# Kernel tuning notes

Measured on AMD Instinct MI355X. Metric: run time of the kernel, lower is better.

## Reference

```python
import jax, jax.numpy as jnp
import numpy as np

T, B, D, H = 1024, 64, 128, 256


def setup_inputs() -> dict:
    key = jax.random.key(0)
    ks = jax.random.split(key, 12)
    k = 1.0 / np.sqrt(H)  # torch LSTMCell init bound
    u = lambda kk, shape: jax.random.uniform(kk, shape, jnp.float32, -k, k)
    inputs = jax.random.normal(ks[0], (T, B, D), jnp.float32)
    hx = jnp.zeros((2, B, H), jnp.float32)
    cx = jnp.zeros((2, B, H), jnp.float32)
    return {
        'inputs': inputs, 'hx': hx, 'cx': cx,
        'Wih_f': u(ks[1], (4 * H, D)), 'Whh_f': u(ks[2], (4 * H, H)),
        'bih_f': u(ks[3], (4 * H,)), 'bhh_f': u(ks[4], (4 * H,)),
        'Wih_r': u(ks[5], (4 * H, D)), 'Whh_r': u(ks[6], (4 * H, H)),
        'bih_r': u(ks[7], (4 * H,)), 'bhh_r': u(ks[8], (4 * H,)),
    }


def _lstm_scan(x, h0, c0, Wih, Whh, bih, bhh, reverse):
    # Batch all input projections up front: [T,B,4H]
    gx = jnp.einsum('tbd,gd->tbg', x, Wih) + (bih + bhh)

    def step(carry, g):
        h, c = carry
        gates = g + h @ Whh.T  # [B,4H]
        i, f, gg, o = jnp.split(gates, 4, axis=-1)  # torch gate order i,f,g,o
        i = jax.nn.sigmoid(i)
        f = jax.nn.sigmoid(f)
        gg = jnp.tanh(gg)
        o = jax.nn.sigmoid(o)
        c = f * c + i * gg
        h = o * jnp.tanh(c)
        return (h, c), h

    # reverse=True scans back-to-front but emits outputs in original time
    # order, matching flip -> loop -> flip in the torch code.
    (h, c), ys = jax.lax.scan(step, (h0, c0), gx, reverse=reverse)
    return ys, h, c


def reference(inputs, hx, cx, Wih_f, Whh_f, bih_f, bhh_f,
              Wih_r, Whh_r, bih_r, bhh_r):
    yf, hf, cf = _lstm_scan(inputs, hx[0], cx[0], Wih_f, Whh_f, bih_f, bhh_f, False)
    yr, hr, cr = _lstm_scan(inputs, hx[1], cx[1], Wih_r, Whh_r, bih_r, bhh_r, True)
    out = jnp.concatenate([yf, yr], axis=-1)  # [T,B,2H]
    hy = jnp.stack([hf, hr], 0)  # [2,B,H]
    cy = jnp.stack([cf, cr], 0)
    return out, hy, cy
```

## Files before the change

### kernel.cpp

```cpp
#include <hip/hip_runtime.h>
#include <cstddef>

#define T_STEPS 1024
#define NB      64
#define DIN     128
#define HID     256
#define WPG     16

typedef unsigned short u16;
typedef unsigned int   u32;
typedef unsigned long long u64;
typedef __attribute__((ext_vector_type(8))) short short8;
typedef __attribute__((ext_vector_type(4))) float f32x4;

#define WG_OFF   0u
#define BIAS_OFF 1572864u
#define XB_OFF   1581056u
#define HB_OFF   18358272u
#define FL_OFF   18489344u

#define OUT_MAIN (T_STEPS * NB * 2 * HID)
#define TAIL_H   OUT_MAIN
#define TAIL_C   (OUT_MAIN + 2 * NB * HID)

__device__ __forceinline__ u16 f2bf(float f) {
  unsigned u = __float_as_uint(f);
  return (u16)((u + 0x7fffu + ((u >> 16) & 1u)) >> 16);
}
__device__ __forceinline__ float sigm(float v) { return 1.f / (1.f + __expf(-v)); }
__device__ __forceinline__ float tanh_fast(float x) {
  float e = __expf(-2.f * fabsf(x));
  float r = (1.f - e) / (1.f + e);
  return x < 0.f ? -r : r;
}

__global__ void prep_kernel(const float* __restrict__ x,
                            const float* __restrict__ Wih_f, const float* __restrict__ Whh_f,
                            const float* __restrict__ bih_f, const float* __restrict__ bhh_f,
                            const float* __restrict__ Wih_r, const float* __restrict__ Whh_r,
                            const float* __restrict__ bih_r, const float* __restrict__ bhh_r,
                            const float* __restrict__ hx,
                            u16* __restrict__ Wg, float* __restrict__ bias4,
                            u16* __restrict__ xb, u16* __restrict__ hbuf,
                            u32* __restrict__ flags) {
  const int total = 786432 + 2048 + 8388608 + 32768 + 8192;
  for (int i = blockIdx.x * blockDim.x + threadIdx.x; i < total;
       i += gridDim.x * blockDim.x) {
    if (i < 786432) {
      int d = i / 393216;
      int r = i - d * 393216;
      int rowg = r / 384, k = r - rowg * 384;
      int j = rowg >> 2, q = rowg & 3;
      int g = q * HID + j;
      const float* Wih = d ? Wih_r : Wih_f;
      const float* Whh = d ? Whh_r : Whh_f;
      float v = (k < DIN) ? Wih[g * DIN + k] : Whh[g * HID + (k - DIN)];
      Wg[i] = f2bf(v);
    } else if (i < 786432 + 2048) {
      int r = i - 786432;
      int d = r >> 10, rowg = r & 1023;
      int j = rowg >> 2, q = rowg & 3;
      int g = q * HID + j;
      bias4[r] = d ? (bih_r[g] + bhh_r[g]) : (bih_f[g] + bhh_f[g]);
    } else if (i < 786432 + 2048 + 8388608) {
      int r = i - (786432 + 2048);
      xb[r] = f2bf(x[r]);
    } else if (i < 786432 + 2048 + 8388608 + 32768) {
      int r = i - (786432 + 2048 + 8388608);
      int d = r >> 14, b = (r >> 8) & 63, j = r & 255;
      int grp = d * 4 + (b >> 4), bb = b & 15;
      hbuf[((size_t)(8 + grp) * 16 + bb) * 256 + j] = f2bf(hx[r]);
      hbuf[((size_t)(0 + grp) * 16 + bb) * 256 + j] = 0;
    } else {
      int r = i - (786432 + 2048 + 8388608 + 32768);
      flags[r] = ((r & 1023) == 0) ? (u32)WPG : 0u;
    }
  }
}

#define MFMA __builtin_amdgcn_mfma_f32_16x16x32_bf16
#define ALD64(P) __hip_atomic_load((P), __ATOMIC_RELAXED, __HIP_MEMORY_SCOPE_AGENT)

__global__ __launch_bounds__(256, 1) void lstm_flag(
    const u16* __restrict__ Wg, const float* __restrict__ bias4,
    const u16* __restrict__ xb, const float* __restrict__ cx,
    u16* __restrict__ hbuf, u32* __restrict__ flags,
    float* __restrict__ out) {
  extern __shared__ char smem[];
  u16* wl   = (u16*)smem;
  u16* xsh  = (u16*)(smem + 50176);
  u16* hsh  = (u16*)(smem + 58880);
  float* gl = (float*)(smem + 67328);

  const int tid = threadIdx.x;
  const int bid = blockIdx.x;
  const int grp = bid & 7;
  const int jsl = bid >> 3;
  const int d = grp >> 2, b0 = (grp & 3) * 16;
  const int w = tid >> 6, l = tid & 63;

  {
    const u32* src = (const u32*)(Wg + (size_t)(d * 1024 + jsl * 64) * 384);
    u32* dst = (u32*)wl;
    for (int iu = tid; iu < 64 * 192; iu += 256) {
      int r = iu / 192, c = iu - r * 192;
      dst[r * 196 + c] = src[iu];
    }
  }
  const float bv = bias4[d * 1024 + jsl * 64 + w * 16 + (l & 15)];

  const int eb = tid >> 4, ej = tid & 15;
  const int jglob = jsl * 16 + ej;
  float c_reg = cx[((size_t)d * NB + b0 + eb) * HID + jglob];

  const int xr_row = tid >> 4;
  const int xc = (tid & 15) * 8;
  const int pb = tid >> 4;
  const int cj0 = (tid & 15) * 16;

  { int t0 = d ? 1023 : 0;
    *(uint4*)&xsh[(0 * 16 + xr_row) * 136 + xc] =
        *(const uint4*)&xb[((size_t)t0 * NB + b0 + xr_row) * DIN + xc]; }
  uint4 xv;
  { int t1 = d ? 1022 : 1;
    xv = *(const uint4*)&xb[((size_t)t1 * NB + b0 + xr_row) * DIN + xc]; }
  u64 h0, h1, h2, h3;
  { const u64* hp = (const u64*)(hbuf + ((size_t)(8 + grp) * 16 + pb) * 256 + cj0);
    h0 = ALD64(hp + 0); h1 = ALD64(hp + 1); h2 = ALD64(hp + 2); h3 = ALD64(hp + 3); }
  __syncthreads();

  for (int s = 0; s < T_STEPS; ++s) {
    const int p = s & 1;
    const int t = d ? (1023 - s) : s;

    if (s < 1023) *(uint4*)&xsh[((p ^ 1) * 16 + xr_row) * 136 + xc] = xv;

    f32x4 acc = {bv, bv, bv, bv};
    {
      const u16* xr = &xsh[(p * 16 + (l & 15)) * 136 + (l >> 4) * 8];
      const u16* wr = wl + (size_t)(w * 16 + (l & 15)) * 392 + (l >> 4) * 8;
      acc = MFMA(*(const short8*)(xr + 0),  *(const short8*)(wr + 0),  acc, 0, 0, 0);
      acc = MFMA(*(const short8*)(xr + 32), *(const short8*)(wr + 32), acc, 0, 0, 0);
      acc = MFMA(*(const short8*)(xr + 64), *(const short8*)(wr + 64), acc, 0, 0, 0);
      acc = MFMA(*(const short8*)(xr + 96), *(const short8*)(wr + 96), acc, 0, 0, 0);
    }
    {
      uint4 H0, H1;
      H0.x = (u32)h0; H0.y = (u32)(h0 >> 32); H0.z = (u32)h1; H0.w = (u32)(h1 >> 32);
      H1.x = (u32)h2; H1.y = (u32)(h2 >> 32); H1.z = (u32)h3; H1.w = (u32)(h3 >> 32);
      *(uint4*)&hsh[pb * 264 + cj0] = H0;
      *(uint4*)&hsh[pb * 264 + cj0 + 8] = H1;
    }
    asm volatile("s_waitcnt lgkmcnt(0)" ::: "memory");
    __builtin_amdgcn_s_barrier();

    {
      const u16* hr = &hsh[(l & 15) * 264 + (l >> 4) * 8];
      const u16* wr = wl + (size_t)(w * 16 + (l & 15)) * 392 + 128 + (l >> 4) * 8;
#pragma unroll
      for (int kb = 0; kb < 8; ++kb)
        acc = MFMA(*(const short8*)(hr + 32 * kb), *(const short8*)(wr + 32 * kb),
                   acc, 0, 0, 0);
    }
    {
      int n = w * 16 + (l & 15);
      int m0 = (l >> 4) * 4;
      gl[(m0 + 0) * 68 + n] = acc[0]; gl[(m0 + 1) * 68 + n] = acc[1];
      gl[(m0 + 2) * 68 + n] = acc[2]; gl[(m0 + 3) * 68 + n] = acc[3];
    }
    asm volatile("s_waitcnt lgkmcnt(0)" ::: "memory");
    __builtin_amdgcn_s_barrier();

    f32x4 g4 = *(const f32x4*)&gl[eb * 68 + 4 * ej];
    float ii = sigm(g4[0]), ff = sigm(g4[1]);
    float gg = tanh_fast(g4[2]), oo = sigm(g4[3]);
    float c = ff * c_reg + ii * gg;
    c_reg = c;
    float h = oo * tanh_fast(c);
    u16 hb16 = f2bf(h);
    __hip_atomic_store(hbuf + ((size_t)(p * 8 + grp) * 16 + eb) * 256 + jglob,
                       hb16, __ATOMIC_RELAXED, __HIP_MEMORY_SCOPE_AGENT);
    asm volatile("s_waitcnt vmcnt(0)" ::: "memory");
    __builtin_amdgcn_s_barrier();
    if (tid == 0 && s < 1023)
      __hip_atomic_fetch_add(flags + grp * 1024 + (s + 1), 1u,
                             __ATOMIC_RELAXED, __HIP_MEMORY_SCOPE_AGENT);
    out[((size_t)t * NB + b0 + eb) * (2 * HID) + d * HID + jglob] = h;
    if (s == 1023) {
      out[TAIL_H + ((size_t)d * NB + b0 + eb) * HID + jglob] = h;
      out[TAIL_C + ((size_t)d * NB + b0 + eb) * HID + jglob] = c;
    }
    if (s < 1022) {
      int tn = d ? (1021 - s) : (s + 2);
      xv = *(const uint4*)&xb[((size_t)tn * NB + b0 + xr_row) * DIN + xc];
    }
    if (s < 1023) {
      if (tid == 0) {
        const u32* fp = flags + grp * 1024 + (s + 1);
        while (__hip_atomic_load(fp, __ATOMIC_RELAXED, __HIP_MEMORY_SCOPE_AGENT) < WPG)
          __builtin_amdgcn_s_sleep(1);
      }
      __builtin_amdgcn_s_barrier();
      const u64* hp = (const u64*)(hbuf + ((size_t)(p * 8 + grp) * 16 + pb) * 256 + cj0);
      h0 = ALD64(hp + 0); h1 = ALD64(hp + 1); h2 = ALD64(hp + 2); h3 = ALD64(hp + 3);
    }
  }
}

extern "C" void kernel_launch(void* const* d_in, const int* in_sizes, int n_in,
                              void* d_out, int out_size, void* d_ws, size_t ws_size,
                              hipStream_t stream) {
  const float* x     = (const float*)d_in[0];
  const float* hx    = (const float*)d_in[1];
  const float* cx    = (const float*)d_in[2];
  const float* Wih_f = (const float*)d_in[3];
  const float* Whh_f = (const float*)d_in[4];
  const float* bih_f = (const float*)d_in[5];
  const float* bhh_f = (const float*)d_in[6];
  const float* Wih_r = (const float*)d_in[7];
  const float* Whh_r = (const float*)d_in[8];
  const float* bih_r = (const float*)d_in[9];
  const float* bhh_r = (const float*)d_in[10];
  float* out = (float*)d_out;

  u16* Wg      = (u16*)((char*)d_ws + WG_OFF);
  float* bias4 = (float*)((char*)d_ws + BIAS_OFF);
  u16* xb      = (u16*)((char*)d_ws + XB_OFF);
  u16* hbuf    = (u16*)((char*)d_ws + HB_OFF);
  u32* flags   = (u32*)((char*)d_ws + FL_OFF);

  hipFuncSetAttribute((const void*)lstm_flag,
                      hipFuncAttributeMaxDynamicSharedMemorySize, 86016);

  hipLaunchKernelGGL(prep_kernel, dim3(2048), dim3(256), 0, stream,
                     x, Wih_f, Whh_f, bih_f, bhh_f, Wih_r, Whh_r, bih_r, bhh_r,
                     hx, Wg, bias4, xb, hbuf, flags);
  hipLaunchKernelGGL(lstm_flag, dim3(128), dim3(256), 86016, stream,
                     Wg, bias4, xb, cx, hbuf, flags, out);
}
```

Measured before the change: 2.167 ms.

## Replace flag-counter barrier with step-tagged hidden-state messages in 4-slot ring

Drops the per-step atomic counter flag and its spin-wait by packing a 16-bit step tag next to each bf16 hidden value in a 32-bit word. Consumers poll the tagged values directly from a 4-deep ring buffer and re-read any word whose tag is stale. The gate activation now runs per wave on its own slice of the LDS scratch, which removes one block barrier per step. MFMA accumulation is split into two chains for ILP. The cost is twice the hbuf traffic and a busy-poll loop with no sleep.

```diff
diff --git a/kernel.cpp b/kernel.cpp
--- a/kernel.cpp
+++ b/kernel.cpp
@@ -5,7 +5,6 @@
 #define NB      64
 #define DIN     128
 #define HID     256
-#define WPG     16
 
 typedef unsigned short u16;
 typedef unsigned int   u32;
@@ -17,7 +16,6 @@
 #define BIAS_OFF 1572864u
 #define XB_OFF   1581056u
 #define HB_OFF   18358272u
-#define FL_OFF   18489344u
 
 #define OUT_MAIN (T_STEPS * NB * 2 * HID)
 #define TAIL_H   OUT_MAIN
@@ -41,9 +39,8 @@
                             const float* __restrict__ bih_r, const float* __restrict__ bhh_r,
                             const float* __restrict__ hx,
                             u16* __restrict__ Wg, float* __restrict__ bias4,
-                            u16* __restrict__ xb, u16* __restrict__ hbuf,
-                            u32* __restrict__ flags) {
-  const int total = 786432 + 2048 + 8388608 + 32768 + 8192;
+                            u16* __restrict__ xb, u32* __restrict__ hbuf) {
+  const int total = 786432 + 2048 + 8388608 + 131072;
   for (int i = blockIdx.x * blockDim.x + threadIdx.x; i < total;
        i += gridDim.x * blockDim.x) {
     if (i < 786432) {
@@ -65,27 +62,31 @@
     } else if (i < 786432 + 2048 + 8388608) {
       int r = i - (786432 + 2048);
       xb[r] = f2bf(x[r]);
-    } else if (i < 786432 + 2048 + 8388608 + 32768) {
+    } else {
       int r = i - (786432 + 2048 + 8388608);
-      int d = r >> 14, b = (r >> 8) & 63, j = r & 255;
-      int grp = d * 4 + (b >> 4), bb = b & 15;
-      hbuf[((size_t)(8 + grp) * 16 + bb) * 256 + j] = f2bf(hx[r]);
-      hbuf[((size_t)(0 + grp) * 16 + bb) * 256 + j] = 0;
-    } else {
-      int r = i - (786432 + 2048 + 8388608 + 32768);
-      flags[r] = ((r & 1023) == 0) ? (u32)WPG : 0u;
+      int slot = r >> 15;
+      int rem  = r & 32767;
+      int grp = rem >> 12, bb = (rem >> 8) & 15, j = r & 255;
+      if (slot == 3) {
+        int d = grp >> 2, b = (grp & 3) * 16 + bb;
+        hbuf[r] = (1u << 16) | f2bf(hx[((size_t)d * NB + b) * HID + j]);
+      } else {
+        hbuf[r] = 0u;
+      }
     }
   }
 }
 
 #define MFMA __builtin_amdgcn_mfma_f32_16x16x32_bf16
 #define ALD64(P) __hip_atomic_load((P), __ATOMIC_RELAXED, __HIP_MEMORY_SCOPE_AGENT)
-
-__global__ __launch_bounds__(256, 1) void lstm_flag(
+#define CHK(V, E) if ((((u32)((V) >> 16) & 0xffffu) != wt) || \
+                      (((u32)((V) >> 48) & 0xffffu) != wt)) { \
+    V = ALD64(cbp + (E)); bad = true; }
+
+__global__ __launch_bounds__(256, 1) void lstm_tag4(
     const u16* __restrict__ Wg, const float* __restrict__ bias4,
     const u16* __restrict__ xb, const float* __restrict__ cx,
-    u16* __restrict__ hbuf, u32* __restrict__ flags,
-    float* __restrict__ out) {
+    u32* __restrict__ hbuf, float* __restrict__ out) {
   extern __shared__ char smem[];
   u16* wl   = (u16*)smem;
   u16* xsh  = (u16*)(smem + 50176);
@@ -109,14 +110,16 @@
   }
   const float bv = bias4[d * 1024 + jsl * 64 + w * 16 + (l & 15)];
 
-  const int eb = tid >> 4, ej = tid & 15;
-  const int jglob = jsl * 16 + ej;
+  const int eb = l >> 2, ejl = l & 3;
+  const int jglob = jsl * 16 + w * 4 + ejl;
   float c_reg = cx[((size_t)d * NB + b0 + eb) * HID + jglob];
+  float* glw = gl + w * 320;
 
   const int xr_row = tid >> 4;
   const int xc = (tid & 15) * 8;
   const int pb = tid >> 4;
-  const int cj0 = (tid & 15) * 16;
+  const int js = tid & 15;
+  const int cj0 = js * 16;
 
   { int t0 = d ? 1023 : 0;
     *(uint4*)&xsh[(0 * 16 + xr_row) * 136 + xc] =
@@ -124,30 +127,53 @@
   uint4 xv;
   { int t1 = d ? 1022 : 1;
     xv = *(const uint4*)&xb[((size_t)t1 * NB + b0 + xr_row) * DIN + xc]; }
-  u64 h0, h1, h2, h3;
-  { const u64* hp = (const u64*)(hbuf + ((size_t)(8 + grp) * 16 + pb) * 256 + cj0);
-    h0 = ALD64(hp + 0); h1 = ALD64(hp + 1); h2 = ALD64(hp + 2); h3 = ALD64(hp + 3); }
   __syncthreads();
 
   for (int s = 0; s < T_STEPS; ++s) {
-    const int p = s & 1;
     const int t = d ? (1023 - s) : s;
-
-    if (s < 1023) *(uint4*)&xsh[((p ^ 1) * 16 + xr_row) * 136 + xc] = xv;
-
-    f32x4 acc = {bv, bv, bv, bv};
-    {
-      const u16* xr = &xsh[(p * 16 + (l & 15)) * 136 + (l >> 4) * 8];
+    const int xp = s & 1;
+    const int sr = (s + 3) & 3;
+    const int sw = s & 3;
+    const u32 wt = (u32)(s + 1) & 0xffffu;
+
+    const u64* cbp = (const u64*)(hbuf + (((size_t)(sr * 8 + grp)) * 16 + pb) * 256 + cj0);
+    u64 v0 = ALD64(cbp + 0), v1 = ALD64(cbp + 1), v2 = ALD64(cbp + 2), v3 = ALD64(cbp + 3);
+    u64 v4 = ALD64(cbp + 4), v5 = ALD64(cbp + 5), v6 = ALD64(cbp + 6), v7 = ALD64(cbp + 7);
+
+    if (s < 1023) *(uint4*)&xsh[((xp ^ 1) * 16 + xr_row) * 136 + xc] = xv;
+
+    f32x4 acc0 = {bv, bv, bv, bv}, acc1 = {0.f, 0.f, 0.f, 0.f};
+    {
+      const u16* xr = &xsh[(xp * 16 + (l & 15)) * 136 + (l >> 4) * 8];
       const u16* wr = wl + (size_t)(w * 16 + (l & 15)) * 392 + (l >> 4) * 8;
-      acc = MFMA(*(const short8*)(xr + 0),  *(const short8*)(wr + 0),  acc, 0, 0, 0);
-      acc = MFMA(*(const short8*)(xr + 32), *(const short8*)(wr + 32), acc, 0, 0, 0);
-      acc = MFMA(*(const short8*)(xr + 64), *(const short8*)(wr + 64), acc, 0, 0, 0);
-      acc = MFMA(*(const short8*)(xr + 96), *(const short8*)(wr + 96), acc, 0, 0, 0);
+      acc0 = MFMA(*(const short8*)(xr + 0),  *(const short8*)(wr + 0),  acc0, 0, 0, 0);
+      acc1 = MFMA(*(const short8*)(xr + 32), *(const short8*)(wr + 32), acc1, 0, 0, 0);
+      acc0 = MFMA(*(const short8*)(xr + 64), *(const short8*)(wr + 64), acc0, 0, 0, 0);
+      acc1 = MFMA(*(const short8*)(xr + 96), *(const short8*)(wr + 96), acc1, 0, 0, 0);
+    }
+    if (s < 1022) {
+      int tn = d ? (1021 - s) : (s + 2);
+      xv = *(const uint4*)&xb[((size_t)tn * NB + b0 + xr_row) * DIN + xc];
+    }
+
+    {
+      bool bad = true;
+      while (bad) {
+        bad = false;
+        CHK(v0, 0) CHK(v1, 1) CHK(v2, 2) CHK(v3, 3)
+        CHK(v4, 4) CHK(v5, 5) CHK(v6, 6) CHK(v7, 7)
+      }
     }
     {
       uint4 H0, H1;
-      H0.x = (u32)h0; H0.y = (u32)(h0 >> 32); H0.z = (u32)h1; H0.w = (u32)(h1 >> 32);
-      H1.x = (u32)h2; H1.y = (u32)(h2 >> 32); H1.z = (u32)h3; H1.w = (u32)(h3 >> 32);
+      H0.x = (u32)(u16)v0 | ((u32)(u16)(v0 >> 32) << 16);
+      H0.y = (u32)(u16)v1 | ((u32)(u16)(v1 >> 32) << 16);
+      H0.z = (u32)(u16)v2 | ((u32)(u16)(v2 >> 32) << 16);
+      H0.w = (u32)(u16)v3 | ((u32)(u16)(v3 >> 32) << 16);
+      H1.x = (u32)(u16)v4 | ((u32)(u16)(v4 >> 32) << 16);
+      H1.y = (u32)(u16)v5 | ((u32)(u16)(v5 >> 32) << 16);
+      H1.z = (u32)(u16)v6 | ((u32)(u16)(v6 >> 32) << 16);
+      H1.w = (u32)(u16)v7 | ((u32)(u16)(v7 >> 32) << 16);
       *(uint4*)&hsh[pb * 264 + cj0] = H0;
       *(uint4*)&hsh[pb * 264 + cj0 + 8] = H1;
     }
@@ -158,52 +184,39 @@
       const u16* hr = &hsh[(l & 15) * 264 + (l >> 4) * 8];
       const u16* wr = wl + (size_t)(w * 16 + (l & 15)) * 392 + 128 + (l >> 4) * 8;
 #pragma unroll
-      for (int kb = 0; kb < 8; ++kb)
-        acc = MFMA(*(const short8*)(hr + 32 * kb), *(const short8*)(wr + 32 * kb),
-                   acc, 0, 0, 0);
-    }
-    {
-      int n = w * 16 + (l & 15);
+      for (int kb = 0; kb < 8; kb += 2) {
+        acc0 = MFMA(*(const short8*)(hr + 32 * kb), *(const short8*)(wr + 32 * kb),
+                    acc0, 0, 0, 0);
+        acc1 = MFMA(*(const short8*)(hr + 32 * (kb + 1)), *(const short8*)(wr + 32 * (kb + 1)),
+                    acc1, 0, 0, 0);
+      }
+    }
+    acc0 = acc0 + acc1;
+    {
+      int n = l & 15;
       int m0 = (l >> 4) * 4;
-      gl[(m0 + 0) * 68 + n] = acc[0]; gl[(m0 + 1) * 68 + n] = acc[1];
-      gl[(m0 + 2) * 68 + n] = acc[2]; gl[(m0 + 3) * 68 + n] = acc[3];
+      glw[(m0 + 0) * 20 + n] = acc0[0]; glw[(m0 + 1) * 20 + n] = acc0[1];
+      glw[(m0 + 2) * 20 + n] = acc0[2]; glw[(m0 + 3) * 20 + n] = acc0[3];
     }
     asm volatile("s_waitcnt lgkmcnt(0)" ::: "memory");
+
+    {
+      f32x4 g4 = *(const f32x4*)&glw[eb * 20 + ejl * 4];
+      float ii = sigm(g4[0]), ff = sigm(g4[1]);
+      float gg = tanh_fast(g4[2]), oo = sigm(g4[3]);
+      float c = ff * c_reg + ii * gg;
+      c_reg = c;
+      float h = oo * tanh_fast(c);
+      u32 msg = ((u32)((s + 2) & 0xffff) << 16) | f2bf(h);
+      __hip_atomic_store(hbuf + (((size_t)(sw * 8 + grp)) * 16 + eb) * 256 + jglob,
+                         msg, __ATOMIC_RELAXED, __HIP_MEMORY_SCOPE_AGENT);
+      out[((size_t)t * NB + b0 + eb) * (2 * HID) + d * HID + jglob] = h;
+      if (s == 1023) {
+        out[TAIL_H + ((size_t)d * NB + b0 + eb) * HID + jglob] = h;
+        out[TAIL_C + ((size_t)d * NB + b0 + eb) * HID + jglob] = c;
+      }
+    }
     __builtin_amdgcn_s_barrier();
-
-    f32x4 g4 = *(const f32x4*)&gl[eb * 68 + 4 * ej];
-    float ii = sigm(g4[0]), ff = sigm(g4[1]);
-    float gg = tanh_fast(g4[2]), oo = sigm(g4[3]);
-    float c = ff * c_reg + ii * gg;
-    c_reg = c;
-    float h = oo * tanh_fast(c);
-    u16 hb16 = f2bf(h);
-    __hip_atomic_store(hbuf + ((size_t)(p * 8 + grp) * 16 + eb) * 256 + jglob,
-                       hb16, __ATOMIC_RELAXED, __HIP_MEMORY_SCOPE_AGENT);
-    asm volatile("s_waitcnt vmcnt(0)" ::: "memory");
-    __builtin_amdgcn_s_barrier();
-    if (tid == 0 && s < 1023)
-      __hip_atomic_fetch_add(flags + grp * 1024 + (s + 1), 1u,
-                             __ATOMIC_RELAXED, __HIP_MEMORY_SCOPE_AGENT);
-    out[((size_t)t * NB + b0 + eb) * (2 * HID) + d * HID + jglob] = h;
-    if (s == 1023) {
-      out[TAIL_H + ((size_t)d * NB + b0 + eb) * HID + jglob] = h;
-      out[TAIL_C + ((size_t)d * NB + b0 + eb) * HID + jglob] = c;
-    }
-    if (s < 1022) {
-      int tn = d ? (1021 - s) : (s + 2);
-      xv = *(const uint4*)&xb[((size_t)tn * NB + b0 + xr_row) * DIN + xc];
-    }
-    if (s < 1023) {
-      if (tid == 0) {
-        const u32* fp = flags + grp * 1024 + (s + 1);
-        while (__hip_atomic_load(fp, __ATOMIC_RELAXED, __HIP_MEMORY_SCOPE_AGENT) < WPG)
-          __builtin_amdgcn_s_sleep(1);
-      }
-      __builtin_amdgcn_s_barrier();
-      const u64* hp = (const u64*)(hbuf + ((size_t)(p * 8 + grp) * 16 + pb) * 256 + cj0);
-      h0 = ALD64(hp + 0); h1 = ALD64(hp + 1); h2 = ALD64(hp + 2); h3 = ALD64(hp + 3);
-    }
   }
 }
 
@@ -226,15 +239,14 @@
   u16* Wg      = (u16*)((char*)d_ws + WG_OFF);
   float* bias4 = (float*)((char*)d_ws + BIAS_OFF);
   u16* xb      = (u16*)((char*)d_ws + XB_OFF);
-  u16* hbuf    = (u16*)((char*)d_ws + HB_OFF);
-  u32* flags   = (u32*)((char*)d_ws + FL_OFF);
-
-  hipFuncSetAttribute((const void*)lstm_flag,
+  u32* hbuf    = (u32*)((char*)d_ws + HB_OFF);
+
+  hipFuncSetAttribute((const void*)lstm_tag4,
                       hipFuncAttributeMaxDynamicSharedMemorySize, 86016);
 
   hipLaunchKernelGGL(prep_kernel, dim3(2048), dim3(256), 0, stream,
                      x, Wih_f, Whh_f, bih_f, bhh_f, Wih_r, Whh_r, bih_r, bhh_r,
-                     hx, Wg, bias4, xb, hbuf, flags);
-  hipLaunchKernelGGL(lstm_flag, dim3(128), dim3(256), 86016, stream,
-                     Wg, bias4, xb, cx, hbuf, flags, out);
-}
+                     hx, Wg, bias4, xb, hbuf);
+  hipLaunchKernelGGL(lstm_tag4, dim3(128), dim3(256), 86016, stream,
+                     Wg, bias4, xb, cx, hbuf, out);
+}
```

New measurement: 4.226 ms. +95.0%, slower.

## Add runtime-probed fast sync path using sc0 loads and per-block step counters

Applied to the files above, without the earlier changes.

At kernel start, blocks in each group run a two-round write/read probe to test whether plain stores become visible to peers through sc0 loads. If every block passes, the recurrence uses plain stores for h, a per-block step counter in place of a shared atomic fetch_add, and a spin that reads all 16 counters with vector sc0 loads and no sleep. h is then read back with two dwordx4 sc0 loads. The intent is to shorten the per-step cross-block handoff latency. The cost is a startup probe and a reliance on cache-coherence behaviour that the probe may not fully guarantee.

```diff
diff --git a/kernel.cpp b/kernel.cpp
--- a/kernel.cpp
+++ b/kernel.cpp
@@ -12,12 +12,17 @@
 typedef unsigned long long u64;
 typedef __attribute__((ext_vector_type(8))) short short8;
 typedef __attribute__((ext_vector_type(4))) float f32x4;
+typedef __attribute__((ext_vector_type(4))) unsigned int u32x4;
 
 #define WG_OFF   0u
 #define BIAS_OFF 1572864u
 #define XB_OFF   1581056u
 #define HB_OFF   18358272u
 #define FL_OFF   18489344u
+#define TST_OFF  18522112u
+#define PRE_OFF  18530304u
+#define OKK_OFF  18530560u
+#define FF_OFF   18531072u
 
 #define OUT_MAIN (T_STEPS * NB * 2 * HID)
 #define TAIL_H   OUT_MAIN
@@ -32,6 +37,12 @@
   float e = __expf(-2.f * fabsf(x));
   float r = (1.f - e) / (1.f + e);
   return x < 0.f ? -r : r;
+}
+__device__ __forceinline__ u32 ld_sc0(const u32* p) {
+  u32 v;
+  asm volatile("global_load_dword %0, %1, off sc0\n\ts_waitcnt vmcnt(0)"
+               : "=&v"(v) : "v"(p) : "memory");
+  return v;
 }
 
 __global__ void prep_kernel(const float* __restrict__ x,
@@ -42,8 +53,8 @@
                             const float* __restrict__ hx,
                             u16* __restrict__ Wg, float* __restrict__ bias4,
                             u16* __restrict__ xb, u16* __restrict__ hbuf,
-                            u32* __restrict__ flags) {
-  const int total = 786432 + 2048 + 8388608 + 32768 + 8192;
+                            u32* __restrict__ flags, u32* __restrict__ aux) {
+  const int total = 786432 + 2048 + 8388608 + 32768 + 8192 + 2368;
   for (int i = blockIdx.x * blockDim.x + threadIdx.x; i < total;
        i += gridDim.x * blockDim.x) {
     if (i < 786432) {
@@ -71,9 +82,11 @@
       int grp = d * 4 + (b >> 4), bb = b & 15;
       hbuf[((size_t)(8 + grp) * 16 + bb) * 256 + j] = f2bf(hx[r]);
       hbuf[((size_t)(0 + grp) * 16 + bb) * 256 + j] = 0;
-    } else {
+    } else if (i < 786432 + 2048 + 8388608 + 32768 + 8192) {
       int r = i - (786432 + 2048 + 8388608 + 32768);
       flags[r] = ((r & 1023) == 0) ? (u32)WPG : 0u;
+    } else {
+      aux[i - (786432 + 2048 + 8388608 + 32768 + 8192)] = 0u;
     }
   }
 }
@@ -81,10 +94,12 @@
 #define MFMA __builtin_amdgcn_mfma_f32_16x16x32_bf16
 #define ALD64(P) __hip_atomic_load((P), __ATOMIC_RELAXED, __HIP_MEMORY_SCOPE_AGENT)
 
-__global__ __launch_bounds__(256, 1) void lstm_flag(
+__global__ __launch_bounds__(256, 1) void lstm_hyb(
     const u16* __restrict__ Wg, const float* __restrict__ bias4,
     const u16* __restrict__ xb, const float* __restrict__ cx,
     u16* __restrict__ hbuf, u32* __restrict__ flags,
+    u32* __restrict__ tst, u32* __restrict__ pre,
+    u32* __restrict__ okk, u32* __restrict__ ff,
     float* __restrict__ out) {
   extern __shared__ char smem[];
   u16* wl   = (u16*)smem;
@@ -98,6 +113,54 @@
   const int jsl = bid >> 3;
   const int d = grp >> 2, b0 = (grp & 3) * 16;
   const int w = tid >> 6, l = tid & 63;
+
+  int fast;
+  {
+    volatile int* lflag = (volatile int*)gl;
+    if (tid == 0) lflag[0] = 0;
+    __syncthreads();
+    for (int rnd = 0; rnd < 2; ++rnd) {
+      u32 base = 0xA5000000u + (u32)rnd * 0x01000000u;
+      if (tid < 16) tst[bid * 16 + tid] = base ^ (u32)(bid * 131 + tid * 7);
+      asm volatile("s_waitcnt vmcnt(0)" ::: "memory");
+      __syncthreads();
+      if (tid == 0) {
+        __hip_atomic_fetch_add(pre + grp * 8 + rnd, 1u, __ATOMIC_RELAXED, __HIP_MEMORY_SCOPE_AGENT);
+        while (__hip_atomic_load(pre + grp * 8 + rnd, __ATOMIC_RELAXED, __HIP_MEMORY_SCOPE_AGENT) < WPG)
+          __builtin_amdgcn_s_sleep(1);
+      }
+      __syncthreads();
+      {
+        int peer = tid >> 4, word = tid & 15;
+        int pbid = peer * 8 + grp;
+        u32 v = ld_sc0(tst + pbid * 16 + word);
+        if (v != (base ^ (u32)(pbid * 131 + word * 7))) lflag[0] = 1;
+      }
+      __syncthreads();
+      if (tid == 0) {
+        __hip_atomic_fetch_add(pre + grp * 8 + 2 + rnd, 1u, __ATOMIC_RELAXED, __HIP_MEMORY_SCOPE_AGENT);
+        while (__hip_atomic_load(pre + grp * 8 + 2 + rnd, __ATOMIC_RELAXED, __HIP_MEMORY_SCOPE_AGENT) < WPG)
+          __builtin_amdgcn_s_sleep(1);
+      }
+      __syncthreads();
+    }
+    if (tid == 0) {
+      __hip_atomic_store(okk + grp * 16 + jsl, lflag[0] ? 1u : 2u,
+                         __ATOMIC_RELAXED, __HIP_MEMORY_SCOPE_AGENT);
+      asm volatile("s_waitcnt vmcnt(0)" ::: "memory");
+      __hip_atomic_fetch_add(pre + grp * 8 + 4, 1u, __ATOMIC_RELAXED, __HIP_MEMORY_SCOPE_AGENT);
+      while (__hip_atomic_load(pre + grp * 8 + 4, __ATOMIC_RELAXED, __HIP_MEMORY_SCOPE_AGENT) < WPG)
+        __builtin_amdgcn_s_sleep(1);
+      u32 all2 = 1;
+      for (int i2 = 0; i2 < 16; ++i2)
+        if (__hip_atomic_load(okk + grp * 16 + i2, __ATOMIC_RELAXED, __HIP_MEMORY_SCOPE_AGENT) != 2u)
+          all2 = 0;
+      lflag[1] = (int)all2;
+    }
+    __syncthreads();
+    fast = lflag[1];
+    __syncthreads();
+  }
 
   {
     const u32* src = (const u32*)(Wg + (size_t)(d * 1024 + jsl * 64) * 384);
@@ -172,19 +235,24 @@
     __builtin_amdgcn_s_barrier();
 
     f32x4 g4 = *(const f32x4*)&gl[eb * 68 + 4 * ej];
-    float ii = sigm(g4[0]), ff = sigm(g4[1]);
+    float ii = sigm(g4[0]), ffg = sigm(g4[1]);
     float gg = tanh_fast(g4[2]), oo = sigm(g4[3]);
-    float c = ff * c_reg + ii * gg;
+    float c = ffg * c_reg + ii * gg;
     c_reg = c;
     float h = oo * tanh_fast(c);
     u16 hb16 = f2bf(h);
-    __hip_atomic_store(hbuf + ((size_t)(p * 8 + grp) * 16 + eb) * 256 + jglob,
-                       hb16, __ATOMIC_RELAXED, __HIP_MEMORY_SCOPE_AGENT);
+    {
+      u16* hp = hbuf + ((size_t)(p * 8 + grp) * 16 + eb) * 256 + jglob;
+      if (fast) *hp = hb16;
+      else __hip_atomic_store(hp, hb16, __ATOMIC_RELAXED, __HIP_MEMORY_SCOPE_AGENT);
+    }
     asm volatile("s_waitcnt vmcnt(0)" ::: "memory");
     __builtin_amdgcn_s_barrier();
-    if (tid == 0 && s < 1023)
-      __hip_atomic_fetch_add(flags + grp * 1024 + (s + 1), 1u,
-                             __ATOMIC_RELAXED, __HIP_MEMORY_SCOPE_AGENT);
+    if (tid == 0 && s < 1023) {
+      if (fast) ff[grp * 16 + jsl] = (u32)(s + 1);
+      else __hip_atomic_fetch_add(flags + grp * 1024 + (s + 1), 1u,
+                                  __ATOMIC_RELAXED, __HIP_MEMORY_SCOPE_AGENT);
+    }
     out[((size_t)t * NB + b0 + eb) * (2 * HID) + d * HID + jglob] = h;
     if (s == 1023) {
       out[TAIL_H + ((size_t)d * NB + b0 + eb) * HID + jglob] = h;
@@ -196,13 +264,50 @@
     }
     if (s < 1023) {
       if (tid == 0) {
-        const u32* fp = flags + grp * 1024 + (s + 1);
-        while (__hip_atomic_load(fp, __ATOMIC_RELAXED, __HIP_MEMORY_SCOPE_AGENT) < WPG)
-          __builtin_amdgcn_s_sleep(1);
+        const u32 wantv = (u32)(s + 1);
+        if (fast) {
+          const u32* fl = ff + grp * 16;
+          while (1) {
+            u32x4 a, b, c2, d2;
+            asm volatile(
+                "global_load_dwordx4 %0, %4, off sc0\n\t"
+                "global_load_dwordx4 %1, %4, off offset:16 sc0\n\t"
+                "global_load_dwordx4 %2, %4, off offset:32 sc0\n\t"
+                "global_load_dwordx4 %3, %4, off offset:48 sc0\n\t"
+                "s_waitcnt vmcnt(0)"
+                : "=&v"(a), "=&v"(b), "=&v"(c2), "=&v"(d2)
+                : "v"(fl) : "memory");
+            u32 mn = a[0];
+#pragma unroll
+            for (int q2 = 1; q2 < 4; ++q2) mn = mn < a[q2] ? mn : a[q2];
+#pragma unroll
+            for (int q2 = 0; q2 < 4; ++q2) { mn = mn < b[q2] ? mn : b[q2];
+              mn = mn < c2[q2] ? mn : c2[q2]; mn = mn < d2[q2] ? mn : d2[q2]; }
+            if (mn >= wantv) break;
+          }
+        } else {
+          const u32* fp = flags + grp * 1024 + (s + 1);
+          while (__hip_atomic_load(fp, __ATOMIC_RELAXED, __HIP_MEMORY_SCOPE_AGENT) < WPG)
+            __builtin_amdgcn_s_sleep(1);
+        }
       }
       __builtin_amdgcn_s_barrier();
-      const u64* hp = (const u64*)(hbuf + ((size_t)(p * 8 + grp) * 16 + pb) * 256 + cj0);
-      h0 = ALD64(hp + 0); h1 = ALD64(hp + 1); h2 = ALD64(hp + 2); h3 = ALD64(hp + 3);
+      if (fast) {
+        const u16* hp = hbuf + ((size_t)(p * 8 + grp) * 16 + pb) * 256 + cj0;
+        u32x4 lo, hi;
+        asm volatile(
+            "global_load_dwordx4 %0, %2, off sc0\n\t"
+            "global_load_dwordx4 %1, %2, off offset:16 sc0\n\t"
+            "s_waitcnt vmcnt(0)"
+            : "=&v"(lo), "=&v"(hi) : "v"(hp) : "memory");
+        h0 = (u64)lo[0] | ((u64)lo[1] << 32);
+        h1 = (u64)lo[2] | ((u64)lo[3] << 32);
+        h2 = (u64)hi[0] | ((u64)hi[1] << 32);
+        h3 = (u64)hi[2] | ((u64)hi[3] << 32);
+      } else {
+        const u64* hp = (const u64*)(hbuf + ((size_t)(p * 8 + grp) * 16 + pb) * 256 + cj0);
+        h0 = ALD64(hp + 0); h1 = ALD64(hp + 1); h2 = ALD64(hp + 2); h3 = ALD64(hp + 3);
+      }
     }
   }
 }
@@ -228,13 +333,17 @@
   u16* xb      = (u16*)((char*)d_ws + XB_OFF);
   u16* hbuf    = (u16*)((char*)d_ws + HB_OFF);
   u32* flags   = (u32*)((char*)d_ws + FL_OFF);
-
-  hipFuncSetAttribute((const void*)lstm_flag,
+  u32* tst     = (u32*)((char*)d_ws + TST_OFF);
+  u32* pre     = (u32*)((char*)d_ws + PRE_OFF);
+  u32* okk     = (u32*)((char*)d_ws + OKK_OFF);
+  u32* ff      = (u32*)((char*)d_ws + FF_OFF);
+
+  hipFuncSetAttribute((const void*)lstm_hyb,
                       hipFuncAttributeMaxDynamicSharedMemorySize, 86016);
 
   hipLaunchKernelGGL(prep_kernel, dim3(2048), dim3(256), 0, stream,
                      x, Wih_f, Whh_f, bih_f, bhh_f, Wih_r, Whh_r, bih_r, bhh_r,
-                     hx, Wg, bias4, xb, hbuf, flags);
-  hipLaunchKernelGGL(lstm_flag, dim3(128), dim3(256), 86016, stream,
-                     Wg, bias4, xb, cx, hbuf, flags, out);
-}
+                     hx, Wg, bias4, xb, hbuf, flags, tst);
+  hipLaunchKernelGGL(lstm_hyb, dim3(128), dim3(256), 86016, stream,
+                     Wg, bias4, xb, cx, hbuf, flags, tst, pre, okk, ff, out);
+}
```

Result: slower. 2.236 ms (+3.2%).

## Keep weights in registers, use per-block step flags polled by all threads

Applied to the files above, without the earlier changes.

Weight fragments now stay in VGPRs for the whole recurrence instead of being staged in LDS and re-read every step. The gate reshuffle goes through a per-wave LDS region, which removes one workgroup barrier per step. The atomic-counter flag per step is replaced by one monotonically increasing step flag per block. Every thread polls all 16 flags of its group with vector loads and takes a min, with no sleep and no barrier after the spin. This is meant to shorten the per-step critical path of the serial recurrence, at the cost of heavier polling traffic and more register pressure.

```diff
diff --git a/kernel.cpp b/kernel.cpp
--- a/kernel.cpp
+++ b/kernel.cpp
@@ -5,7 +5,6 @@
 #define NB      64
 #define DIN     128
 #define HID     256
-#define WPG     16
 
 typedef unsigned short u16;
 typedef unsigned int   u32;
@@ -43,7 +42,7 @@
                             u16* __restrict__ Wg, float* __restrict__ bias4,
                             u16* __restrict__ xb, u16* __restrict__ hbuf,
                             u32* __restrict__ flags) {
-  const int total = 786432 + 2048 + 8388608 + 32768 + 8192;
+  const int total = 786432 + 2048 + 8388608 + 32768 + 128;
   for (int i = blockIdx.x * blockDim.x + threadIdx.x; i < total;
        i += gridDim.x * blockDim.x) {
     if (i < 786432) {
@@ -72,25 +71,25 @@
       hbuf[((size_t)(8 + grp) * 16 + bb) * 256 + j] = f2bf(hx[r]);
       hbuf[((size_t)(0 + grp) * 16 + bb) * 256 + j] = 0;
     } else {
-      int r = i - (786432 + 2048 + 8388608 + 32768);
-      flags[r] = ((r & 1023) == 0) ? (u32)WPG : 0u;
+      flags[i - (786432 + 2048 + 8388608 + 32768)] = 0u;
     }
   }
 }
 
 #define MFMA __builtin_amdgcn_mfma_f32_16x16x32_bf16
 #define ALD64(P) __hip_atomic_load((P), __ATOMIC_RELAXED, __HIP_MEMORY_SCOPE_AGENT)
-
-__global__ __launch_bounds__(256, 1) void lstm_flag(
+#define MN2(F) { u32 a_ = (u32)(F), b_ = (u32)((F) >> 32); \
+                 mn = mn < a_ ? mn : a_; mn = mn < b_ ? mn : b_; }
+
+__global__ __launch_bounds__(256, 1) void lstm_r13(
     const u16* __restrict__ Wg, const float* __restrict__ bias4,
     const u16* __restrict__ xb, const float* __restrict__ cx,
     u16* __restrict__ hbuf, u32* __restrict__ flags,
     float* __restrict__ out) {
   extern __shared__ char smem[];
-  u16* wl   = (u16*)smem;
-  u16* xsh  = (u16*)(smem + 50176);
-  u16* hsh  = (u16*)(smem + 58880);
-  float* gl = (float*)(smem + 67328);
+  u16* xsh  = (u16*)smem;
+  u16* hsh  = (u16*)(smem + 8704);
+  float* gl = (float*)(smem + 17152);
 
   const int tid = threadIdx.x;
   const int bid = blockIdx.x;
@@ -99,19 +98,26 @@
   const int d = grp >> 2, b0 = (grp & 3) * 16;
   const int w = tid >> 6, l = tid & 63;
 
-  {
-    const u32* src = (const u32*)(Wg + (size_t)(d * 1024 + jsl * 64) * 384);
-    u32* dst = (u32*)wl;
-    for (int iu = tid; iu < 64 * 192; iu += 256) {
-      int r = iu / 192, c = iu - r * 192;
-      dst[r * 196 + c] = src[iu];
-    }
-  }
+  const u16* wgb = Wg + ((size_t)(d * 1024 + jsl * 64 + w * 16 + (l & 15))) * 384
+                      + (l >> 4) * 8;
+  short8 Wx0 = *(const short8*)(wgb + 0);
+  short8 Wx1 = *(const short8*)(wgb + 32);
+  short8 Wx2 = *(const short8*)(wgb + 64);
+  short8 Wx3 = *(const short8*)(wgb + 96);
+  short8 Wh0 = *(const short8*)(wgb + 128);
+  short8 Wh1 = *(const short8*)(wgb + 160);
+  short8 Wh2 = *(const short8*)(wgb + 192);
+  short8 Wh3 = *(const short8*)(wgb + 224);
+  short8 Wh4 = *(const short8*)(wgb + 256);
+  short8 Wh5 = *(const short8*)(wgb + 288);
+  short8 Wh6 = *(const short8*)(wgb + 320);
+  short8 Wh7 = *(const short8*)(wgb + 352);
   const float bv = bias4[d * 1024 + jsl * 64 + w * 16 + (l & 15)];
 
-  const int eb = tid >> 4, ej = tid & 15;
-  const int jglob = jsl * 16 + ej;
+  const int eb = l >> 2, ejl = l & 3;
+  const int jglob = jsl * 16 + w * 4 + ejl;
   float c_reg = cx[((size_t)d * NB + b0 + eb) * HID + jglob];
+  float* glw = gl + w * 320;
 
   const int xr_row = tid >> 4;
   const int xc = (tid & 15) * 8;
@@ -138,11 +144,10 @@
     f32x4 acc = {bv, bv, bv, bv};
     {
       const u16* xr = &xsh[(p * 16 + (l & 15)) * 136 + (l >> 4) * 8];
-      const u16* wr = wl + (size_t)(w * 16 + (l & 15)) * 392 + (l >> 4) * 8;
-      acc = MFMA(*(const short8*)(xr + 0),  *(const short8*)(wr + 0),  acc, 0, 0, 0);
-      acc = MFMA(*(const short8*)(xr + 32), *(const short8*)(wr + 32), acc, 0, 0, 0);
-      acc = MFMA(*(const short8*)(xr + 64), *(const short8*)(wr + 64), acc, 0, 0, 0);
-      acc = MFMA(*(const short8*)(xr + 96), *(const short8*)(wr + 96), acc, 0, 0, 0);
+      acc = MFMA(*(const short8*)(xr + 0),  Wx0, acc, 0, 0, 0);
+      acc = MFMA(*(const short8*)(xr + 32), Wx1, acc, 0, 0, 0);
+      acc = MFMA(*(const short8*)(xr + 64), Wx2, acc, 0, 0, 0);
+      acc = MFMA(*(const short8*)(xr + 96), Wx3, acc, 0, 0, 0);
     }
     {
       uint4 H0, H1;
@@ -156,51 +161,61 @@
 
     {
       const u16* hr = &hsh[(l & 15) * 264 + (l >> 4) * 8];
-      const u16* wr = wl + (size_t)(w * 16 + (l & 15)) * 392 + 128 + (l >> 4) * 8;
-#pragma unroll
-      for (int kb = 0; kb < 8; ++kb)
-        acc = MFMA(*(const short8*)(hr + 32 * kb), *(const short8*)(wr + 32 * kb),
-                   acc, 0, 0, 0);
-    }
-    {
-      int n = w * 16 + (l & 15);
+      acc = MFMA(*(const short8*)(hr + 0),   Wh0, acc, 0, 0, 0);
+      acc = MFMA(*(const short8*)(hr + 32),  Wh1, acc, 0, 0, 0);
+      acc = MFMA(*(const short8*)(hr + 64),  Wh2, acc, 0, 0, 0);
+      acc = MFMA(*(const short8*)(hr + 96),  Wh3, acc, 0, 0, 0);
+      acc = MFMA(*(const short8*)(hr + 128), Wh4, acc, 0, 0, 0);
+      acc = MFMA(*(const short8*)(hr + 160), Wh5, acc, 0, 0, 0);
+      acc = MFMA(*(const short8*)(hr + 192), Wh6, acc, 0, 0, 0);
+      acc = MFMA(*(const short8*)(hr + 224), Wh7, acc, 0, 0, 0);
+    }
+    {
+      int n = l & 15;
       int m0 = (l >> 4) * 4;
-      gl[(m0 + 0) * 68 + n] = acc[0]; gl[(m0 + 1) * 68 + n] = acc[1];
-      gl[(m0 + 2) * 68 + n] = acc[2]; gl[(m0 + 3) * 68 + n] = acc[3];
+      glw[(m0 + 0) * 20 + n] = acc[0]; glw[(m0 + 1) * 20 + n] = acc[1];
+      glw[(m0 + 2) * 20 + n] = acc[2]; glw[(m0 + 3) * 20 + n] = acc[3];
     }
     asm volatile("s_waitcnt lgkmcnt(0)" ::: "memory");
-    __builtin_amdgcn_s_barrier();
-
-    f32x4 g4 = *(const f32x4*)&gl[eb * 68 + 4 * ej];
-    float ii = sigm(g4[0]), ff = sigm(g4[1]);
-    float gg = tanh_fast(g4[2]), oo = sigm(g4[3]);
-    float c = ff * c_reg + ii * gg;
-    c_reg = c;
-    float h = oo * tanh_fast(c);
-    u16 hb16 = f2bf(h);
-    __hip_atomic_store(hbuf + ((size_t)(p * 8 + grp) * 16 + eb) * 256 + jglob,
-                       hb16, __ATOMIC_RELAXED, __HIP_MEMORY_SCOPE_AGENT);
+
+    float h, c;
+    {
+      f32x4 g4 = *(const f32x4*)&glw[eb * 20 + ejl * 4];
+      float ii = sigm(g4[0]), ffg = sigm(g4[1]);
+      float gg = tanh_fast(g4[2]), oo = sigm(g4[3]);
+      c = ffg * c_reg + ii * gg;
+      c_reg = c;
+      h = oo * tanh_fast(c);
+      __hip_atomic_store(hbuf + ((size_t)(p * 8 + grp) * 16 + eb) * 256 + jglob,
+                         f2bf(h), __ATOMIC_RELAXED, __HIP_MEMORY_SCOPE_AGENT);
+      out[((size_t)t * NB + b0 + eb) * (2 * HID) + d * HID + jglob] = h;
+      if (s == 1023) {
+        out[TAIL_H + ((size_t)d * NB + b0 + eb) * HID + jglob] = h;
+        out[TAIL_C + ((size_t)d * NB + b0 + eb) * HID + jglob] = c;
+      }
+    }
     asm volatile("s_waitcnt vmcnt(0)" ::: "memory");
     __builtin_amdgcn_s_barrier();
-    if (tid == 0 && s < 1023)
-      __hip_atomic_fetch_add(flags + grp * 1024 + (s + 1), 1u,
-                             __ATOMIC_RELAXED, __HIP_MEMORY_SCOPE_AGENT);
-    out[((size_t)t * NB + b0 + eb) * (2 * HID) + d * HID + jglob] = h;
-    if (s == 1023) {
-      out[TAIL_H + ((size_t)d * NB + b0 + eb) * HID + jglob] = h;
-      out[TAIL_C + ((size_t)d * NB + b0 + eb) * HID + jglob] = c;
-    }
-    if (s < 1022) {
-      int tn = d ? (1021 - s) : (s + 2);
-      xv = *(const uint4*)&xb[((size_t)tn * NB + b0 + xr_row) * DIN + xc];
-    }
+
     if (s < 1023) {
-      if (tid == 0) {
-        const u32* fp = flags + grp * 1024 + (s + 1);
-        while (__hip_atomic_load(fp, __ATOMIC_RELAXED, __HIP_MEMORY_SCOPE_AGENT) < WPG)
-          __builtin_amdgcn_s_sleep(1);
+      if (tid == 0)
+        __hip_atomic_store(flags + grp * 16 + jsl, (u32)(s + 1),
+                           __ATOMIC_RELAXED, __HIP_MEMORY_SCOPE_AGENT);
+      if (s < 1022) {
+        int tn = d ? (1021 - s) : (s + 2);
+        xv = *(const uint4*)&xb[((size_t)tn * NB + b0 + xr_row) * DIN + xc];
       }
-      __builtin_amdgcn_s_barrier();
+      {
+        const u64* fl = (const u64*)(flags + grp * 16);
+        const u32 want = (u32)(s + 1);
+        while (1) {
+          u64 f0 = ALD64(fl + 0), f1 = ALD64(fl + 1), f2 = ALD64(fl + 2), f3 = ALD64(fl + 3);
+          u64 f4 = ALD64(fl + 4), f5 = ALD64(fl + 5), f6 = ALD64(fl + 6), f7 = ALD64(fl + 7);
+          u32 mn = 0xffffffffu;
+          MN2(f0) MN2(f1) MN2(f2) MN2(f3) MN2(f4) MN2(f5) MN2(f6) MN2(f7)
+          if (mn >= want) break;
+        }
+      }
       const u64* hp = (const u64*)(hbuf + ((size_t)(p * 8 + grp) * 16 + pb) * 256 + cj0);
       h0 = ALD64(hp + 0); h1 = ALD64(hp + 1); h2 = ALD64(hp + 2); h3 = ALD64(hp + 3);
     }
@@ -229,12 +244,12 @@
   u16* hbuf    = (u16*)((char*)d_ws + HB_OFF);
   u32* flags   = (u32*)((char*)d_ws + FL_OFF);
 
-  hipFuncSetAttribute((const void*)lstm_flag,
+  hipFuncSetAttribute((const void*)lstm_r13,
                       hipFuncAttributeMaxDynamicSharedMemorySize, 86016);
 
   hipLaunchKernelGGL(prep_kernel, dim3(2048), dim3(256), 0, stream,
                      x, Wih_f, Whh_f, bih_f, bhh_f, Wih_r, Whh_r, bih_r, bhh_r,
                      hx, Wg, bias4, xb, hbuf, flags);
-  hipLaunchKernelGGL(lstm_flag, dim3(128), dim3(256), 86016, stream,
+  hipLaunchKernelGGL(lstm_r13, dim3(128), dim3(256), 86016, stream,
                      Wg, bias4, xb, cx, hbuf, flags, out);
 }
```

Result: slower. 3.165 ms (+46.1%).
